# Optimization experiments

Measured on AMD Instinct MI355X. Metric: run time of the kernel, lower is better.

Reference implementation:

```python
import jax, jax.numpy as jnp
import numpy as np

B, L, DM = 1, 512, 768
DS, DC, EX = 64, 4, 2
DI = EX * DM            # d_inner = 1536
DR = DM // 16           # dt_rank = 48


def setup_inputs() -> dict:
    key = jax.random.key(0)
    ks = jax.random.split(key, 12)
    s = 0.02
    inp = {
        "x": jax.random.normal(ks[0], (B, L, DM), dtype=jnp.float32),
        "ln_w": jnp.ones((DM,), jnp.float32),
        "ln_b": jnp.zeros((DM,), jnp.float32),
        "in_proj_w": jax.random.normal(ks[1], (2 * DI, DM), jnp.float32) * s,
        "conv_w": jax.random.normal(ks[2], (DI, 1, DC), jnp.float32) * s,
        "conv_b": jnp.zeros((DI,), jnp.float32),
        "x_proj_w": jax.random.normal(ks[3], (DR + 2 * DS, DI), jnp.float32) * s,
        "dt_proj_w": jax.random.normal(ks[4], (DI, DR), jnp.float32) * s,
        "dt_proj_b": jax.random.normal(ks[5], (DI,), jnp.float32) * s,
        "A_log": jnp.log(jnp.broadcast_to(jnp.arange(1, DS + 1, dtype=jnp.float32), (DI, DS))),
        "D": jnp.ones((DI,), jnp.float32),
        "out_proj_w": jax.random.normal(ks[6], (DM, DI), jnp.float32) * s,
    }
    return inp


def _layernorm(x, w, b, eps=1e-5):
    mu = jnp.mean(x, axis=-1, keepdims=True)
    var = jnp.mean((x - mu) ** 2, axis=-1, keepdims=True)
    return (x - mu) * jax.lax.rsqrt(var + eps) * w + b


def _causal_depthwise_conv(x, w, b):
    # x: [B, L, DI] -> conv over time, depthwise, causal (left pad DC-1)
    xc = jnp.transpose(x, (0, 2, 1))  # [B, DI, L]
    y = jax.lax.conv_general_dilated(
        xc, w, window_strides=(1,), padding=[(DC - 1, 0)],
        dimension_numbers=("NCH", "OIH", "NCH"), feature_group_count=DI)
    y = y + b[None, :, None]
    return jnp.transpose(y, (0, 2, 1))  # [B, L, DI]


def _selective_scan(deltaA, deltaB_u, C):
    # deltaA, deltaB_u: [B, L, DI, DS]; C: [B, L, DS]
    dA = jnp.transpose(deltaA, (1, 0, 2, 3))
    dBu = jnp.transpose(deltaB_u, (1, 0, 2, 3))
    Ct = jnp.transpose(C, (1, 0, 2))
    s0 = jnp.zeros(deltaA.shape[:1] + deltaA.shape[2:], deltaA.dtype).transpose(0, 1, 2)
    s0 = jnp.zeros((deltaA.shape[0], deltaA.shape[2], deltaA.shape[3]), deltaA.dtype)

    def step(s, inp):
        dA_t, dBu_t, C_t = inp
        s = dA_t * s + dBu_t                      # [B, DI, DS]
        y = jnp.einsum("bdn,bn->bd", s, C_t)      # [B, DI]
        return s, y

    _, ys = jax.lax.scan(step, s0, (dA, dBu, Ct))
    return jnp.transpose(ys, (1, 0, 2))           # [B, L, DI]


def reference(x, ln_w, ln_b, in_proj_w, conv_w, conv_b, x_proj_w,
              dt_proj_w, dt_proj_b, A_log, D, out_proj_w):
    residual = x
    h = _layernorm(x, ln_w, ln_b)
    xz = jnp.einsum("bld,ed->ble", h, in_proj_w)  # [B, L, 2*DI]
    x_in, z = jnp.split(xz, 2, axis=-1)
    x_in = jax.nn.silu(_causal_depthwise_conv(x_in, conv_w, conv_b))
    x_dbl = jnp.einsum("bld,ed->ble", x_in, x_proj_w)  # [B, L, DR+2*DS]
    dt, Bm, Cm = jnp.split(x_dbl, [DR, DR + DS], axis=-1)
    dt = jax.nn.softplus(jnp.einsum("blr,dr->bld", dt, dt_proj_w) + dt_proj_b)  # [B,L,DI]
    A = -jnp.exp(A_log)                                 # [DI, DS]
    deltaA = jnp.exp(dt[..., None] * A)                 # [B, L, DI, DS]
    deltaB_u = dt[..., None] * Bm[:, :, None, :] * x_in[..., None]
    y = _selective_scan(deltaA, deltaB_u, Cm)           # [B, L, DI]
    y = y + x_in * D
    y = y * jax.nn.silu(z)
    out = jnp.einsum("bld,ed->ble", y, out_proj_w)      # [B, L, DM]
    return residual + out
```

## Files before the change

kernel.cpp:

```cpp
#include <hip/hip_runtime.h>
#include <hip/hip_bf16.h>
#include <math.h>

#define L_SEQ 512
#define DM 768
#define DI 1536
#define DS 64
#define DC 4
#define DR 48
#define NXD 176
#define NC 8
#define TC 64

typedef __attribute__((ext_vector_type(8))) short short8;
typedef __attribute__((ext_vector_type(4))) float float4v;

#define NWI (2 * DI * DM)
#define NWX (NXD * DI)
#define NWDT (DI * DR)
#define NWO (DM * DI)
#define NXZ (L_SEQ * 2 * DI)
#define NXDBL (L_SEQ * NXD)
#define NXR (L_SEQ * DM)

#define B_LN 512
#define B_WI (NWI / 1024)
#define B_WX (NWX / 1024)
#define B_WDT (NWDT / 1024)
#define B_WO (NWO / 1024)
#define B_XZ (NXZ / 1024)
#define B_XD (NXDBL / 1024)
#define B_CP (NXR / 1024)
#define PREP_GRID (B_LN + B_WI + B_WX + B_WDT + B_WO + B_XZ + B_XD + B_CP)

__device__ __forceinline__ float bp_add(float p, int addr) {
  return p + __int_as_float(__builtin_amdgcn_ds_bpermute(addr, __float_as_int(p)));
}
__device__ __forceinline__ float lane_read(float v, int t) {
  return __int_as_float(__builtin_amdgcn_readlane(__float_as_int(v), t));
}
__device__ __forceinline__ short f2bf(float v) {
  __hip_bfloat16 h = __float2bfloat16(v);
  return *reinterpret_cast<short*>(&h);
}
__device__ __forceinline__ short8 cvt8f(const float* p, bool valid) {
  float4 u = *(const float4*)(p);
  float4 v = *(const float4*)(p + 4);
  short8 r;
  r[0] = f2bf(u.x); r[1] = f2bf(u.y); r[2] = f2bf(u.z); r[3] = f2bf(u.w);
  r[4] = f2bf(v.x); r[5] = f2bf(v.y); r[6] = f2bf(v.z); r[7] = f2bf(v.w);
  if (!valid) r = (short8)0;
  return r;
}
__device__ __forceinline__ void atomic_addf(float* p, float v) {
  __hip_atomic_fetch_add(p, v, __ATOMIC_RELAXED, __HIP_MEMORY_SCOPE_AGENT);
}

__device__ __forceinline__ void cvt_blk(const float* __restrict__ s,
                                        short* __restrict__ d, int b) {
  int i = b * 1024 + threadIdx.x * 4;
  float4 v = *(const float4*)(s + i);
  short4 o; o.x = f2bf(v.x); o.y = f2bf(v.y); o.z = f2bf(v.z); o.w = f2bf(v.w);
  *(short4*)(d + i) = o;
}
__global__ __launch_bounds__(256) void prep(
    const float* __restrict__ x, const float* __restrict__ lnw,
    const float* __restrict__ lnb, short* __restrict__ h,
    const float* __restrict__ wi, short* __restrict__ wib,
    const float* __restrict__ wx, short* __restrict__ wxb,
    const float* __restrict__ wdt, short* __restrict__ wdtb,
    const float* __restrict__ wo, short* __restrict__ wob,
    float* __restrict__ xz, float* __restrict__ xdbl, float* __restrict__ out) {
  int b = blockIdx.x;
  if (b < B_LN) {
    int l = b, tid = threadIdx.x;
    const float* xr = x + l * DM;
    float s = 0.f, s2 = 0.f;
    for (int i = tid; i < DM; i += 256) { float t = xr[i]; s += t; s2 += t * t; }
#pragma unroll
    for (int off = 32; off; off >>= 1) { s += __shfl_xor(s, off); s2 += __shfl_xor(s2, off); }
    __shared__ float ls[4], ls2[4];
    int wid = tid >> 6, lane = tid & 63;
    if (lane == 0) { ls[wid] = s; ls2[wid] = s2; }
    __syncthreads();
    s = ls[0] + ls[1] + ls[2] + ls[3];
    s2 = ls2[0] + ls2[1] + ls2[2] + ls2[3];
    float mean = s * (1.f / DM);
    float var = s2 * (1.f / DM) - mean * mean;
    float rstd = rsqrtf(var + 1e-5f);
    for (int i = tid; i < DM; i += 256)
      h[l * DM + i] = f2bf((xr[i] - mean) * rstd * lnw[i] + lnb[i]);
    return;
  }
  b -= B_LN;
  if (b < B_WI) { cvt_blk(wi, wib, b); return; }
  b -= B_WI;
  if (b < B_WX) { cvt_blk(wx, wxb, b); return; }
  b -= B_WX;
  if (b < B_WDT) { cvt_blk(wdt, wdtb, b); return; }
  b -= B_WDT;
  if (b < B_WO) { cvt_blk(wo, wob, b); return; }
  b -= B_WO;
  if (b < B_XZ) {
    int i = b * 1024 + threadIdx.x * 4;
    *(float4*)(xz + i) = make_float4(0.f, 0.f, 0.f, 0.f);
    return;
  }
  b -= B_XZ;
  if (b < B_XD) {
    int i = b * 1024 + threadIdx.x * 4;
    *(float4*)(xdbl + i) = make_float4(0.f, 0.f, 0.f, 0.f);
    return;
  }
  b -= B_XD;
  {
    int i = b * 1024 + threadIdx.x * 4;
    *(float4*)(out + i) = *(const float4*)(x + i);
  }
}

__global__ __launch_bounds__(256) void gemm_bf16(const short* __restrict__ A, int lda,
                                                 const short* __restrict__ B,
                                                 float* __restrict__ C,
                                                 int N, int K) {
  int lane = threadIdx.x & 63, w = threadIdx.x >> 6;
  int fr = lane & 15, koff = (lane >> 4) * 8;
  int mbase = blockIdx.y * 64 + (w & 1) * 32;
  int nbase = blockIdx.x * 64 + (w >> 1) * 32;
  int kchunk = K / gridDim.z;
  int kbeg = blockIdx.z * kchunk, kend = kbeg + kchunk;
  int nr0 = nbase + fr;      if (nr0 > N - 1) nr0 = N - 1;
  int nr1 = nbase + 16 + fr; if (nr1 > N - 1) nr1 = N - 1;
  const short* pA0 = A + (size_t)(mbase + fr) * lda + koff;
  const short* pA1 = pA0 + (size_t)16 * lda;
  const short* pB0 = B + (size_t)nr0 * K + koff;
  const short* pB1 = B + (size_t)nr1 * K + koff;
  float4v acc00 = (float4v){0.f,0.f,0.f,0.f}, acc01 = acc00;
  float4v acc10 = acc00, acc11 = acc00;
  short8 a0 = *(const short8*)(pA0 + kbeg);
  short8 a1 = *(const short8*)(pA1 + kbeg);
  short8 b0 = *(const short8*)(pB0 + kbeg);
  short8 b1 = *(const short8*)(pB1 + kbeg);
  for (int k0 = kbeg; k0 < kend; k0 += 32) {
    short8 ca0 = a0, ca1 = a1, cb0 = b0, cb1 = b1;
    int kn = (k0 + 32 < kend) ? k0 + 32 : kbeg;
    a0 = *(const short8*)(pA0 + kn);
    a1 = *(const short8*)(pA1 + kn);
    b0 = *(const short8*)(pB0 + kn);
    b1 = *(const short8*)(pB1 + kn);
    acc00 = __builtin_amdgcn_mfma_f32_16x16x32_bf16(ca0, cb0, acc00, 0, 0, 0);
    acc01 = __builtin_amdgcn_mfma_f32_16x16x32_bf16(ca0, cb1, acc01, 0, 0, 0);
    acc10 = __builtin_amdgcn_mfma_f32_16x16x32_bf16(ca1, cb0, acc10, 0, 0, 0);
    acc11 = __builtin_amdgcn_mfma_f32_16x16x32_bf16(ca1, cb1, acc11, 0, 0, 0);
  }
  int col0 = nbase + fr, col1 = nbase + 16 + fr;
  int rb = mbase + (lane >> 4) * 4;
#pragma unroll
  for (int r = 0; r < 4; ++r) {
    if (col0 < N) {
      atomic_addf(&C[(size_t)(rb + r) * N + col0], acc00[r]);
      atomic_addf(&C[(size_t)(rb + 16 + r) * N + col0], acc10[r]);
    }
    if (col1 < N) {
      atomic_addf(&C[(size_t)(rb + r) * N + col1], acc01[r]);
      atomic_addf(&C[(size_t)(rb + 16 + r) * N + col1], acc11[r]);
    }
  }
}

__global__ __launch_bounds__(256) void dtp_gemm(const float* __restrict__ Axd,
                                                const short* __restrict__ Bw,
                                                float* __restrict__ dt,
                                                const float* __restrict__ bias) {
  int lane = threadIdx.x & 63, w = threadIdx.x >> 6;
  int fr = lane & 15, koff = (lane >> 4) * 8;
  int mbase = blockIdx.y * 64 + (w & 1) * 32;
  int nbase = blockIdx.x * 64 + (w >> 1) * 32;
  const float* pA0 = Axd + (size_t)(mbase + fr) * NXD;
  const float* pA1 = pA0 + (size_t)16 * NXD;
  const short* pB0 = Bw + (size_t)(nbase + fr) * DR;
  const short* pB1 = Bw + (size_t)(nbase + 16 + fr) * DR;
  float4v acc00 = (float4v){0.f,0.f,0.f,0.f}, acc01 = acc00;
  float4v acc10 = acc00, acc11 = acc00;
#pragma unroll
  for (int k0 = 0; k0 < 64; k0 += 32) {
    bool valid = (k0 + koff) < DR;
    int off = valid ? k0 + koff : 0;
    short8 a0 = cvt8f(pA0 + off, valid);
    short8 a1 = cvt8f(pA1 + off, valid);
    short8 b0 = *(const short8*)(pB0 + off);
    short8 b1 = *(const short8*)(pB1 + off);
    if (!valid) { b0 = (short8)0; b1 = (short8)0; }
    acc00 = __builtin_amdgcn_mfma_f32_16x16x32_bf16(a0, b0, acc00, 0, 0, 0);
    acc01 = __builtin_amdgcn_mfma_f32_16x16x32_bf16(a0, b1, acc01, 0, 0, 0);
    acc10 = __builtin_amdgcn_mfma_f32_16x16x32_bf16(a1, b0, acc10, 0, 0, 0);
    acc11 = __builtin_amdgcn_mfma_f32_16x16x32_bf16(a1, b1, acc11, 0, 0, 0);
  }
  int col0 = nbase + fr, col1 = nbase + 16 + fr;
  float bi0 = bias[col0], bi1 = bias[col1];
  int rb = mbase + (lane >> 4) * 4;
#pragma unroll
  for (int r = 0; r < 4; ++r) {
    float v0 = acc00[r] + bi0, v1 = acc01[r] + bi1;
    float v2 = acc10[r] + bi0, v3 = acc11[r] + bi1;
    v0 = (v0 > 20.f) ? v0 : log1pf(__expf(v0));
    v1 = (v1 > 20.f) ? v1 : log1pf(__expf(v1));
    v2 = (v2 > 20.f) ? v2 : log1pf(__expf(v2));
    v3 = (v3 > 20.f) ? v3 : log1pf(__expf(v3));
    dt[(size_t)(rb + r) * DI + col0] = v0;
    dt[(size_t)(rb + r) * DI + col1] = v1;
    dt[(size_t)(rb + 16 + r) * DI + col0] = v2;
    dt[(size_t)(rb + 16 + r) * DI + col1] = v3;
  }
}

__global__ __launch_bounds__(256) void conv_silu_kernel(const float* __restrict__ xz,
                                                        const float* __restrict__ cw,
                                                        const float* __restrict__ cb,
                                                        float* __restrict__ xc,
                                                        short* __restrict__ xcb) {
  int idx = blockIdx.x * 256 + threadIdx.x;
  if (idx >= L_SEQ * DI) return;
  int l = idx / DI, d = idx - l * DI;
  float acc = cb[d];
#pragma unroll
  for (int j = 0; j < DC; ++j) {
    int ll = l - (DC - 1) + j;
    if (ll >= 0) acc = fmaf(xz[(size_t)ll * (2 * DI) + d], cw[d * DC + j], acc);
  }
  float sig = 1.f / (1.f + __expf(-acc));
  float v = acc * sig;
  xc[idx] = v;
  xcb[idx] = f2bf(v);
}

__global__ __launch_bounds__(256) void scan_p1(const float* __restrict__ dt,
                                               const float* __restrict__ xc,
                                               const float* __restrict__ xdbl,
                                               const float* __restrict__ A_log,
                                               float* __restrict__ send,
                                               float* __restrict__ dts) {
  int lane = threadIdx.x & 63;
  int wid = threadIdx.x >> 6;
  int pair = blockIdx.x * 4 + wid;
  int c = __builtin_amdgcn_readfirstlane(pair / DI);
  int d = __builtin_amdgcn_readfirstlane(pair - (pair / DI) * DI);
  float A = -__expf(A_log[(size_t)d * DS + lane]);
  int l0 = c * TC;
  float dtv = dt[(size_t)(l0 + lane) * DI + d];
  float xv  = xc[(size_t)(l0 + lane) * DI + d];
  const float* pB = xdbl + (size_t)l0 * NXD + DR + lane;
  float s = 0.f;
#pragma unroll 8
  for (int t = 0; t < TC; ++t) {
    float dt_c = lane_read(dtv, t);
    float x_c  = lane_read(xv, t);
    float B_c  = pB[(size_t)t * NXD];
    float dA = __expf(dt_c * A);
    s = fmaf(dA, s, dt_c * x_c * B_c);
  }
  float dsum = dtv;
  dsum = bp_add(dsum, (lane ^ 1) << 2);  dsum = bp_add(dsum, (lane ^ 2) << 2);
  dsum = bp_add(dsum, (lane ^ 4) << 2);  dsum = bp_add(dsum, (lane ^ 8) << 2);
  dsum = bp_add(dsum, (lane ^ 16) << 2); dsum = bp_add(dsum, (lane ^ 32) << 2);
  send[((size_t)c * DI + d) * DS + lane] = s;
  if (lane == 0) dts[c * DI + d] = dsum;
}

__global__ __launch_bounds__(256) void scan_p2(const float* __restrict__ send,
                                               const float* __restrict__ dts,
                                               const float* __restrict__ A_log,
                                               float* __restrict__ sinit) {
  int lane = threadIdx.x & 63;
  int wid = threadIdx.x >> 6;
  int d = __builtin_amdgcn_readfirstlane(blockIdx.x * 4 + wid);
  float A = -__expf(A_log[(size_t)d * DS + lane]);
  float s = 0.f;
  for (int c = 1; c < NC; ++c) {
    float P = __expf(A * dts[(c - 1) * DI + d]);
    s = fmaf(P, s, send[((size_t)(c - 1) * DI + d) * DS + lane]);
    sinit[((size_t)c * DI + d) * DS + lane] = s;
  }
}

__global__ __launch_bounds__(256) void scan_p3(const float* __restrict__ dt,
                                               const float* __restrict__ xc,
                                               const float* __restrict__ xdbl,
                                               const float* __restrict__ A_log,
                                               const float* __restrict__ Dv,
                                               const float* __restrict__ xz,
                                               const float* __restrict__ sinit,
                                               short* __restrict__ y) {
  __shared__ float Pb[4][16][66];
  int lane = threadIdx.x & 63;
  int wid = threadIdx.x >> 6;
  int pair = blockIdx.x * 4 + wid;
  int c = __builtin_amdgcn_readfirstlane(pair / DI);
  int d = __builtin_amdgcn_readfirstlane(pair - (pair / DI) * DI);
  float A = -__expf(A_log[(size_t)d * DS + lane]);
  float Dd = Dv[d];
  int l0 = c * TC;
  float dtv = dt[(size_t)(l0 + lane) * DI + d];
  float xv  = xc[(size_t)(l0 + lane) * DI + d];
  float zv  = xz[(size_t)(l0 + lane) * (2 * DI) + DI + d];
  float s = (c == 0) ? 0.f : sinit[((size_t)c * DI + d) * DS + lane];
  const float* pB = xdbl + (size_t)l0 * NXD + DR + lane;
  float yv = 0.f;
#pragma unroll
  for (int sb = 0; sb < 4; ++sb) {
    float P[16];
#pragma unroll
    for (int j = 0; j < 16; ++j) {
      int t = sb * 16 + j;
      float dt_c = lane_read(dtv, t);
      float x_c  = lane_read(xv, t);
      float B_c  = pB[(size_t)t * NXD];
      float C_c  = pB[(size_t)t * NXD + DS];
      float dA = __expf(dt_c * A);
      s = fmaf(dA, s, dt_c * x_c * B_c);
      P[j] = s * C_c;
    }
#pragma unroll
    for (int j = 0; j < 16; ++j) Pb[wid][j][lane] = P[j];
    int t4 = lane >> 2, q = lane & 3;
    const float* row = &Pb[wid][t4][q * 16];
    float part = 0.f;
#pragma unroll
    for (int k = 0; k < 8; ++k) {
      float2 v2 = *(const float2*)(row + 2 * k);
      part += v2.x + v2.y;
    }
    part = bp_add(part, (lane ^ 1) << 2);
    part = bp_add(part, (lane ^ 2) << 2);
    float got = __int_as_float(
        __builtin_amdgcn_ds_bpermute((lane & 15) << 4, __float_as_int(part)));
    yv = ((lane >> 4) == sb) ? got : yv;
  }
  float sig = 1.f / (1.f + __expf(-zv));
  y[(size_t)(l0 + lane) * DI + d] = f2bf((yv + xv * Dd) * (zv * sig));
}

extern "C" void kernel_launch(void* const* d_in, const int* in_sizes, int n_in,
                              void* d_out, int out_size, void* d_ws, size_t ws_size,
                              hipStream_t stream) {
  const float* x         = (const float*)d_in[0];
  const float* ln_w      = (const float*)d_in[1];
  const float* ln_b      = (const float*)d_in[2];
  const float* in_proj_w = (const float*)d_in[3];
  const float* conv_w    = (const float*)d_in[4];
  const float* conv_b    = (const float*)d_in[5];
  const float* x_proj_w  = (const float*)d_in[6];
  const float* dt_proj_w = (const float*)d_in[7];
  const float* dt_proj_b = (const float*)d_in[8];
  const float* A_log     = (const float*)d_in[9];
  const float* Dv        = (const float*)d_in[10];
  const float* out_proj_w= (const float*)d_in[11];
  float* out = (float*)d_out;

  float* ws = (float*)d_ws;
  float* xz    = ws;
  float* xconv = xz + NXZ;
  float* xdbl  = xconv + 786432;
  float* dtb   = xdbl + NXDBL;
  float* send  = dtb + 786432;
  float* dts   = send + 688128;
  float* sinit = dts + 10752;
  float* fend  = sinit + 786432;
  short* h_bf   = (short*)fend;
  short* wi_bf  = h_bf + NXR;
  short* wx_bf  = wi_bf + NWI;
  short* wdt_bf = wx_bf + NWX;
  short* wo_bf  = wdt_bf + NWDT;
  short* xc_bf  = wo_bf + NWO;
  short* y_bf   = xc_bf + (L_SEQ * DI);

  prep<<<PREP_GRID, 256, 0, stream>>>(x, ln_w, ln_b, h_bf,
                                      in_proj_w, wi_bf, x_proj_w, wx_bf,
                                      dt_proj_w, wdt_bf, out_proj_w, wo_bf,
                                      xz, xdbl, out);

  gemm_bf16<<<dim3(2 * DI / 64, L_SEQ / 64, 3), 256, 0, stream>>>(
      h_bf, DM, wi_bf, xz, 2 * DI, DM);

  conv_silu_kernel<<<(L_SEQ * DI) / 256, 256, 0, stream>>>(xz, conv_w, conv_b,
                                                           xconv, xc_bf);

  gemm_bf16<<<dim3((NXD + 63) / 64, L_SEQ / 64, 16), 256, 0, stream>>>(
      xc_bf, DI, wx_bf, xdbl, NXD, DI);

  dtp_gemm<<<dim3(DI / 64, L_SEQ / 64), 256, 0, stream>>>(
      xdbl, wdt_bf, dtb, dt_proj_b);

  scan_p1<<<((NC - 1) * DI) / 4, 256, 0, stream>>>(dtb, xconv, xdbl, A_log, send, dts);
  scan_p2<<<DI / 4, 256, 0, stream>>>(send, dts, A_log, sinit);
  scan_p3<<<(NC * DI) / 4, 256, 0, stream>>>(dtb, xconv, xdbl, A_log, Dv, xz, sinit, y_bf);

  gemm_bf16<<<dim3(DM / 64, L_SEQ / 64, 6), 256, 0, stream>>>(
      y_bf, DI, wo_bf, out, DM, DI);
}
```

Baseline: 208.9 us.

## Replace atomic split-K accumulation with direct stores, partial buffers and fused residual

The GEMMs no longer accumulate with float atomics into pre-zeroed buffers. in_proj and out_proj now run without split-K and store directly, with the residual add fused into the out_proj epilogue. x_proj writes 8 partial slabs that a new reduce kernel sums. This removes the zeroing and copy work in prep and the atomic traffic, and the GEMM inner loop now double-buffers 64-wide K steps. The cost is fewer blocks for the large GEMMs (lower parallelism) plus an extra kernel launch and partial-buffer traffic.

```diff
diff --git a/kernel.cpp b/kernel.cpp
--- a/kernel.cpp
+++ b/kernel.cpp
@@ -28,10 +28,7 @@
 #define B_WX (NWX / 1024)
 #define B_WDT (NWDT / 1024)
 #define B_WO (NWO / 1024)
-#define B_XZ (NXZ / 1024)
-#define B_XD (NXDBL / 1024)
-#define B_CP (NXR / 1024)
-#define PREP_GRID (B_LN + B_WI + B_WX + B_WDT + B_WO + B_XZ + B_XD + B_CP)
+#define PREP_GRID (B_LN + B_WI + B_WX + B_WDT + B_WO)
 
 __device__ __forceinline__ float bp_add(float p, int addr) {
   return p + __int_as_float(__builtin_amdgcn_ds_bpermute(addr, __float_as_int(p)));
@@ -52,9 +49,6 @@
   if (!valid) r = (short8)0;
   return r;
 }
-__device__ __forceinline__ void atomic_addf(float* p, float v) {
-  __hip_atomic_fetch_add(p, v, __ATOMIC_RELAXED, __HIP_MEMORY_SCOPE_AGENT);
-}
 
 __device__ __forceinline__ void cvt_blk(const float* __restrict__ s,
                                         short* __restrict__ d, int b) {
@@ -69,8 +63,7 @@
     const float* __restrict__ wi, short* __restrict__ wib,
     const float* __restrict__ wx, short* __restrict__ wxb,
     const float* __restrict__ wdt, short* __restrict__ wdtb,
-    const float* __restrict__ wo, short* __restrict__ wob,
-    float* __restrict__ xz, float* __restrict__ xdbl, float* __restrict__ out) {
+    const float* __restrict__ wo, short* __restrict__ wob) {
   int b = blockIdx.x;
   if (b < B_LN) {
     int l = b, tid = threadIdx.x;
@@ -99,73 +92,79 @@
   b -= B_WX;
   if (b < B_WDT) { cvt_blk(wdt, wdtb, b); return; }
   b -= B_WDT;
-  if (b < B_WO) { cvt_blk(wo, wob, b); return; }
-  b -= B_WO;
-  if (b < B_XZ) {
-    int i = b * 1024 + threadIdx.x * 4;
-    *(float4*)(xz + i) = make_float4(0.f, 0.f, 0.f, 0.f);
-    return;
-  }
-  b -= B_XZ;
-  if (b < B_XD) {
-    int i = b * 1024 + threadIdx.x * 4;
-    *(float4*)(xdbl + i) = make_float4(0.f, 0.f, 0.f, 0.f);
-    return;
-  }
-  b -= B_XD;
-  {
-    int i = b * 1024 + threadIdx.x * 4;
-    *(float4*)(out + i) = *(const float4*)(x + i);
-  }
+  cvt_blk(wo, wob, b);
 }
 
 __global__ __launch_bounds__(256) void gemm_bf16(const short* __restrict__ A, int lda,
                                                  const short* __restrict__ B,
                                                  float* __restrict__ C,
-                                                 int N, int K) {
+                                                 int N, int K,
+                                                 const float* __restrict__ res,
+                                                 int mode) {
   int lane = threadIdx.x & 63, w = threadIdx.x >> 6;
   int fr = lane & 15, koff = (lane >> 4) * 8;
   int mbase = blockIdx.y * 64 + (w & 1) * 32;
   int nbase = blockIdx.x * 64 + (w >> 1) * 32;
   int kchunk = K / gridDim.z;
-  int kbeg = blockIdx.z * kchunk, kend = kbeg + kchunk;
+  int kbeg = blockIdx.z * kchunk;
   int nr0 = nbase + fr;      if (nr0 > N - 1) nr0 = N - 1;
   int nr1 = nbase + 16 + fr; if (nr1 > N - 1) nr1 = N - 1;
-  const short* pA0 = A + (size_t)(mbase + fr) * lda + koff;
+  const short* pA0 = A + (size_t)(mbase + fr) * lda + koff + kbeg;
   const short* pA1 = pA0 + (size_t)16 * lda;
-  const short* pB0 = B + (size_t)nr0 * K + koff;
-  const short* pB1 = B + (size_t)nr1 * K + koff;
+  const short* pB0 = B + (size_t)nr0 * K + koff + kbeg;
+  const short* pB1 = B + (size_t)nr1 * K + koff + kbeg;
   float4v acc00 = (float4v){0.f,0.f,0.f,0.f}, acc01 = acc00;
   float4v acc10 = acc00, acc11 = acc00;
-  short8 a0 = *(const short8*)(pA0 + kbeg);
-  short8 a1 = *(const short8*)(pA1 + kbeg);
-  short8 b0 = *(const short8*)(pB0 + kbeg);
-  short8 b1 = *(const short8*)(pB1 + kbeg);
-  for (int k0 = kbeg; k0 < kend; k0 += 32) {
-    short8 ca0 = a0, ca1 = a1, cb0 = b0, cb1 = b1;
-    int kn = (k0 + 32 < kend) ? k0 + 32 : kbeg;
-    a0 = *(const short8*)(pA0 + kn);
-    a1 = *(const short8*)(pA1 + kn);
-    b0 = *(const short8*)(pB0 + kn);
-    b1 = *(const short8*)(pB1 + kn);
+  short8 a0A = *(const short8*)(pA0);      short8 a1A = *(const short8*)(pA1);
+  short8 b0A = *(const short8*)(pB0);      short8 b1A = *(const short8*)(pB1);
+  short8 a0B = *(const short8*)(pA0 + 32); short8 a1B = *(const short8*)(pA1 + 32);
+  short8 b0B = *(const short8*)(pB0 + 32); short8 b1B = *(const short8*)(pB1 + 32);
+  for (int k0 = 0; k0 < kchunk; k0 += 64) {
+    short8 ca0 = a0A, ca1 = a1A, cb0 = b0A, cb1 = b1A;
+    short8 da0 = a0B, da1 = a1B, db0 = b0B, db1 = b1B;
+    int nA = k0 + 64; if (nA >= kchunk) nA = 0;
+    int nB = k0 + 96; if (nB >= kchunk) nB = 32;
+    a0A = *(const short8*)(pA0 + nA); a1A = *(const short8*)(pA1 + nA);
+    b0A = *(const short8*)(pB0 + nA); b1A = *(const short8*)(pB1 + nA);
+    a0B = *(const short8*)(pA0 + nB); a1B = *(const short8*)(pA1 + nB);
+    b0B = *(const short8*)(pB0 + nB); b1B = *(const short8*)(pB1 + nB);
     acc00 = __builtin_amdgcn_mfma_f32_16x16x32_bf16(ca0, cb0, acc00, 0, 0, 0);
     acc01 = __builtin_amdgcn_mfma_f32_16x16x32_bf16(ca0, cb1, acc01, 0, 0, 0);
     acc10 = __builtin_amdgcn_mfma_f32_16x16x32_bf16(ca1, cb0, acc10, 0, 0, 0);
     acc11 = __builtin_amdgcn_mfma_f32_16x16x32_bf16(ca1, cb1, acc11, 0, 0, 0);
-  }
+    acc00 = __builtin_amdgcn_mfma_f32_16x16x32_bf16(da0, db0, acc00, 0, 0, 0);
+    acc01 = __builtin_amdgcn_mfma_f32_16x16x32_bf16(da0, db1, acc01, 0, 0, 0);
+    acc10 = __builtin_amdgcn_mfma_f32_16x16x32_bf16(da1, db0, acc10, 0, 0, 0);
+    acc11 = __builtin_amdgcn_mfma_f32_16x16x32_bf16(da1, db1, acc11, 0, 0, 0);
+  }
+  float* Cz = C + (size_t)blockIdx.z * (size_t)L_SEQ * (size_t)N;
   int col0 = nbase + fr, col1 = nbase + 16 + fr;
   int rb = mbase + (lane >> 4) * 4;
 #pragma unroll
   for (int r = 0; r < 4; ++r) {
+    size_t o00 = (size_t)(rb + r) * N;
+    size_t o10 = (size_t)(rb + 16 + r) * N;
     if (col0 < N) {
-      atomic_addf(&C[(size_t)(rb + r) * N + col0], acc00[r]);
-      atomic_addf(&C[(size_t)(rb + 16 + r) * N + col0], acc10[r]);
+      float v0 = acc00[r], v1 = acc10[r];
+      if (mode == 2) { v0 += res[o00 + col0]; v1 += res[o10 + col0]; }
+      Cz[o00 + col0] = v0; Cz[o10 + col0] = v1;
     }
     if (col1 < N) {
-      atomic_addf(&C[(size_t)(rb + r) * N + col1], acc01[r]);
-      atomic_addf(&C[(size_t)(rb + 16 + r) * N + col1], acc11[r]);
+      float v0 = acc01[r], v1 = acc11[r];
+      if (mode == 2) { v0 += res[o00 + col1]; v1 += res[o10 + col1]; }
+      Cz[o00 + col1] = v0; Cz[o10 + col1] = v1;
     }
   }
+}
+
+__global__ __launch_bounds__(256) void reduce_add(const float* __restrict__ part,
+                                                  int MN, int splitk,
+                                                  float* __restrict__ out) {
+  int i = blockIdx.x * 256 + threadIdx.x;
+  if (i >= MN) return;
+  float a = 0.f;
+  for (int z = 0; z < splitk; ++z) a += part[(size_t)z * MN + i];
+  out[i] = a;
 }
 
 __global__ __launch_bounds__(256) void dtp_gemm(const float* __restrict__ Axd,
@@ -365,7 +364,8 @@
   float* send  = dtb + 786432;
   float* dts   = send + 688128;
   float* sinit = dts + 10752;
-  float* fend  = sinit + 786432;
+  float* part2 = sinit + 786432;
+  float* fend  = part2 + 720896;
   short* h_bf   = (short*)fend;
   short* wi_bf  = h_bf + NXR;
   short* wx_bf  = wi_bf + NWI;
@@ -376,17 +376,17 @@
 
   prep<<<PREP_GRID, 256, 0, stream>>>(x, ln_w, ln_b, h_bf,
                                       in_proj_w, wi_bf, x_proj_w, wx_bf,
-                                      dt_proj_w, wdt_bf, out_proj_w, wo_bf,
-                                      xz, xdbl, out);
-
-  gemm_bf16<<<dim3(2 * DI / 64, L_SEQ / 64, 3), 256, 0, stream>>>(
-      h_bf, DM, wi_bf, xz, 2 * DI, DM);
+                                      dt_proj_w, wdt_bf, out_proj_w, wo_bf);
+
+  gemm_bf16<<<dim3(2 * DI / 64, L_SEQ / 64, 1), 256, 0, stream>>>(
+      h_bf, DM, wi_bf, xz, 2 * DI, DM, nullptr, 0);
 
   conv_silu_kernel<<<(L_SEQ * DI) / 256, 256, 0, stream>>>(xz, conv_w, conv_b,
                                                            xconv, xc_bf);
 
-  gemm_bf16<<<dim3((NXD + 63) / 64, L_SEQ / 64, 16), 256, 0, stream>>>(
-      xc_bf, DI, wx_bf, xdbl, NXD, DI);
+  gemm_bf16<<<dim3((NXD + 63) / 64, L_SEQ / 64, 8), 256, 0, stream>>>(
+      xc_bf, DI, wx_bf, part2, NXD, DI, nullptr, 0);
+  reduce_add<<<(NXDBL + 255) / 256, 256, 0, stream>>>(part2, NXDBL, 8, xdbl);
 
   dtp_gemm<<<dim3(DI / 64, L_SEQ / 64), 256, 0, stream>>>(
       xdbl, wdt_bf, dtb, dt_proj_b);
@@ -395,6 +395,6 @@
   scan_p2<<<DI / 4, 256, 0, stream>>>(send, dts, A_log, sinit);
   scan_p3<<<(NC * DI) / 4, 256, 0, stream>>>(dtb, xconv, xdbl, A_log, Dv, xz, sinit, y_bf);
 
-  gemm_bf16<<<dim3(DM / 64, L_SEQ / 64, 6), 256, 0, stream>>>(
-      y_bf, DI, wo_bf, out, DM, DI);
-}
+  gemm_bf16<<<dim3(DM / 64, L_SEQ / 64, 1), 256, 0, stream>>>(
+      y_bf, DI, wo_bf, out, DM, DI, x, 2);
+}
```

Measured after the change: 212.4 us. Within noise of the previous version (+1.7%).
